# Performance work log

Measured on AMD Instinct MI355X. Metric: run time of the kernel, lower is better.

Reference implementation:

```python
import jax, jax.numpy as jnp
import numpy as np
from jax import lax

NH, K, V, TOPK = 8, 64, 64, 4  # n_heads, key_size, val_size, SparseAttention top_k(=3+1)
EPS = 1e-7
BN_EPS = 1e-5


def conv1x1(x, w, b):
    # x: [B,C,H,W], w: [O,C] -> [B,O,H,W]
    return jnp.einsum('oc,bchw->bohw', w, x) + b[None, :, None, None]


def conv3x3(x, w, b):
    y = lax.conv_general_dilated(x, w, (1, 1), 'SAME',
                                 dimension_numbers=('NCHW', 'OIHW', 'NCHW'))
    return y + b[None, :, None, None]


def batchnorm(x, g, b):
    # training-mode BN over (N,H,W), biased variance (matches torch BatchNorm2d in train)
    m = jnp.mean(x, axis=(0, 2, 3), keepdims=True)
    v = jnp.var(x, axis=(0, 2, 3), keepdims=True)
    return (x - m) * lax.rsqrt(v + BN_EPS) * g[None, :, None, None] + b[None, :, None, None]


def to_flat(y, d):
    # [B, NH*d, H, W] -> [B*H*W*NH, d]
    B, _, H, W = y.shape
    return y.reshape(B, NH, d, H, W).transpose(0, 3, 4, 1, 2).reshape(B * H * W * NH, d)


def setup_inputs() -> dict:
    key = jax.random.key(0)
    ks = jax.random.split(key, 16)
    L, C, B, H, W = 4, 256, 8, 32, 32
    KH, VH = K * NH, V * NH
    s = 0.02
    return {
        'x': jax.random.normal(ks[0], (B, C, H, W), jnp.float32),
        'kw': jax.random.normal(ks[1], (L, KH, C), jnp.float32) * s,
        'kb': jax.random.normal(ks[2], (L, KH), jnp.float32) * s,
        'qw': jax.random.normal(ks[3], (L, KH, C), jnp.float32) * s,
        'qb': jax.random.normal(ks[4], (L, KH), jnp.float32) * s,
        'vw': jax.random.normal(ks[5], (L, VH, C), jnp.float32) * s,
        'vb': jax.random.normal(ks[6], (L, VH), jnp.float32) * s,
        'ow1': jax.random.normal(ks[7], (L, C, VH, 3, 3), jnp.float32) * s,
        'ob1': jax.random.normal(ks[8], (L, C), jnp.float32) * s,
        'bn_g': jnp.ones((L, C), jnp.float32),
        'bn_b': jnp.zeros((L, C), jnp.float32),
        'ow2': jax.random.normal(ks[9], (L, C, C, 3, 3), jnp.float32) * s,
        'ob2': jax.random.normal(ks[10], (L, C), jnp.float32) * s,
        'gammas': jax.random.normal(ks[11], (L,), jnp.float32),
    }


def reference(x, kw, kb, qw, qb, vw, vb, ow1, ob1, bn_g, bn_b, ow2, ob2, gammas):
    B, C, H, W = x.shape
    L = kw.shape[0]
    temp = jnp.asarray(np.power(K, 0.5), x.dtype)  # concentration=0.5
    keys, vals = [], []
    for l in range(L):  # structurally distinct layers: growing key/val list
        keys.append(to_flat(conv1x1(x, kw[l], kb[l]), K))  # [N,K]
        vals.append(to_flat(conv1x1(x, vw[l], vb[l]), V))  # [N,V]
        q = to_flat(conv1x1(x, qw[l], qb[l]), K)           # [N,K]
        kt = jnp.stack(keys + [jnp.zeros_like(keys[0])], axis=1)  # [N,T,K] zero key appended
        vt = jnp.stack(vals + [jnp.zeros_like(vals[0])], axis=1)  # [N,T,V]
        scores = jnp.einsum('nk,ntk->nt', q / temp, kt)
        attn = jax.nn.softmax(scores, axis=-1)
        T = attn.shape[1]
        if T > TOPK:  # SparseAttention: topk threshold, clamp, renormalize
            delta = lax.top_k(attn, TOPK)[0][:, -1] + EPS
            wgt = jnp.maximum(attn - delta[:, None], 0.0)
            attn = wgt / (jnp.sum(wgt, axis=1, keepdims=True) + EPS)
        o = jnp.einsum('nt,ntv->nv', attn, vt)  # [N,V]
        o = o.reshape(B, H, W, NH * V).transpose(0, 3, 1, 2)  # [B, NH*V, H, W]
        h1 = jax.nn.relu(batchnorm(conv3x3(o, ow1[l], ob1[l]), bn_g[l], bn_b[l]))
        h2 = conv3x3(h1, ow2[l], ob2[l])
        x = x + h2 * gammas[l]
    return x
```

## Files before the change

### kernel.cpp

```cpp
#include <hip/hip_runtime.h>


typedef __attribute__((ext_vector_type(8))) short short8;
typedef __attribute__((ext_vector_type(4))) float f32x4;
typedef __attribute__((ext_vector_type(2))) float f32x2;
typedef __attribute__((ext_vector_type(4))) unsigned short ushort4_t;
typedef __attribute__((ext_vector_type(4))) unsigned int uint4_t;

#define NTOK 65536
#define NPIX 8192

#define PREP_FLAT 7752
#define PREP_W1   (PREP_FLAT + 1024)
#define PREP_W2   (PREP_W1 + 1024)
#define PREP_TOT  (PREP_W2 + 128)

__device__ __forceinline__ float bf2f(unsigned short u) {
  unsigned int v = ((unsigned int)u) << 16;
  float f; __builtin_memcpy(&f, &v, 4); return f;
}
__device__ __forceinline__ unsigned short f2bf(float f) {
  unsigned int u; __builtin_memcpy(&u, &f, 4);
  u = (u + 0x7FFFu + ((u >> 16) & 1u)) >> 16;
  return (unsigned short)u;
}
__device__ __forceinline__ float blo(unsigned int u) {
  unsigned int v = u << 16; float f; __builtin_memcpy(&f, &v, 4); return f;
}
__device__ __forceinline__ float bhi(unsigned int u) {
  unsigned int v = u & 0xFFFF0000u; float f; __builtin_memcpy(&f, &v, 4); return f;
}

__device__ __forceinline__ void gl_lds16(const unsigned short* g, const unsigned short* l) {
  __builtin_amdgcn_global_load_lds(
      (const __attribute__((address_space(1))) unsigned int*)g,
      (__attribute__((address_space(3))) unsigned int*)l, 16, 0, 0);
}

__global__ void k_prep(const float* __restrict__ kw, const float* __restrict__ vw,
                       const float* __restrict__ qw, const float* __restrict__ ow1,
                       const float* __restrict__ ow2, const float* __restrict__ kb,
                       const float* __restrict__ vb, const float* __restrict__ qb,
                       unsigned short* __restrict__ wkqv, unsigned short* __restrict__ w1,
                       unsigned short* __restrict__ w2, float* __restrict__ biascat,
                       unsigned int* __restrict__ opad_u32, unsigned int* __restrict__ h1pad_u32,
                       const float* __restrict__ x_in, float* __restrict__ xacc,
                       unsigned short* __restrict__ xcl) {
  const int bid = blockIdx.x;
  const int tid = threadIdx.x;

  if (bid < PREP_FLAT) {
    long i = (long)bid * 256 + tid;
    if (i < 1572864) {
      int idx = (int)(i & 131071); int sl = (int)(i >> 17); int slot = sl % 3, l = sl / 3;
      const float* s = slot == 0 ? kw : slot == 1 ? vw : qw;
      float v = s[(size_t)l * 131072 + idx];
      if (slot == 2) v *= 0.125f;
      wkqv[i] = f2bf(v);
      return;
    }
    i -= 1572864;
    if (i < 6144) {
      int o = (int)(i & 511); int sl = (int)(i >> 9); int slot = sl % 3, l = sl / 3;
      const float* s = slot == 0 ? kb : slot == 1 ? vb : qb;
      float v = s[l * 512 + o];
      if (slot == 2) v *= 0.125f;
      biascat[i] = v;
      return;
    }
    i -= 6144;
    auto border_pix = [](int pidx) -> size_t {
      const int b = pidx / 132, t = pidx % 132;
      int y, x;
      if (t < 34) { y = 0; x = t; }
      else if (t < 68) { y = 33; x = t - 34; }
      else { const int j = t - 68; y = 1 + (j >> 1); x = (j & 1) * 33; }
      return (size_t)b * 1156 + y * 34 + x;
    };
    if (i < 270336) {
      const int pidx = (int)(i >> 8), c = (int)(i & 255);
      opad_u32[border_pix(pidx) * 256 + c] = 0u;
      return;
    }
    i -= 270336;
    if (i < 135168) {
      const int pidx = (int)(i >> 7), c = (int)(i & 127);
      h1pad_u32[border_pix(pidx) * 128 + c] = 0u;
    }
    return;
  }

  if (bid < PREP_W1) {
    __shared__ unsigned short lds[4608];
    const int m = bid - PREP_FLAT;
    const float* src = ow1 + (size_t)m * 4608;
    #pragma unroll
    for (int k = 0; k < 18; k++) lds[k * 256 + tid] = f2bf(src[k * 256 + tid]);
    __syncthreads();
    unsigned int* dst = (unsigned int*)(w1 + (size_t)m * 4608);
    #pragma unroll
    for (int j = 0; j < 9; j++) {
      const int u = j * 256 + tid;
      const int o = 2 * u;
      const int tap = o >> 9, c = o & 511;
      dst[u] = (unsigned int)lds[c * 9 + tap] |
               ((unsigned int)lds[(c + 1) * 9 + tap] << 16);
    }
    return;
  }

  if (bid < PREP_W2) {
    __shared__ unsigned short lds2[2304];
    const int m = bid - PREP_W1;
    const float* src = ow2 + (size_t)m * 2304;
    #pragma unroll
    for (int k = 0; k < 9; k++) lds2[k * 256 + tid] = f2bf(src[k * 256 + tid]);
    __syncthreads();
    unsigned int* dst = (unsigned int*)(w2 + (size_t)m * 2304);
    #pragma unroll
    for (int j = 0; j < 5; j++) {
      const int u = j * 256 + tid;
      if (u < 1152) {
        const int o = 2 * u;
        const int tap = o >> 8, c = o & 255;
        dst[u] = (unsigned int)lds2[c * 9 + tap] |
                 ((unsigned int)lds2[(c + 1) * 9 + tap] << 16);
      }
    }
    return;
  }

  {
    __shared__ unsigned short t[64][68];
    const int xb = bid - PREP_W2;
    const int hw0 = (xb & 15) * 64, b = xb >> 4;
    for (int cc = 0; cc < 4; cc++) {
      __syncthreads();
      {
        const int px = tid & 63, c = tid >> 6;
        #pragma unroll
        for (int i = 0; i < 16; i++) {
          const size_t idx = ((size_t)b * 256 + cc * 64 + c + i * 4) * 1024 + hw0 + px;
          const float v = x_in[idx];
          xacc[idx] = v;
          t[px][c + i * 4] = f2bf(v);
        }
      }
      __syncthreads();
      {
        const int px = tid >> 2, c0 = (tid & 3) * 16;
        unsigned short* dp = xcl + ((size_t)b * 1024 + hw0 + px) * 256 + cc * 64 + c0;
        short8 v0, v1;
        #pragma unroll
        for (int i = 0; i < 8; i++) { v0[i] = (short)t[px][c0 + i]; v1[i] = (short)t[px][c0 + 8 + i]; }
        *(short8*)dp = v0; *(short8*)(dp + 8) = v1;
      }
    }
  }
}

template<int MODE, int NSTEP, int KDIM, int CIN, int NBUF>
__global__ __launch_bounds__(256) void k_gemm(
    const unsigned short* __restrict__ W,
    const unsigned short* __restrict__ act,
    const float* __restrict__ bias,
    int l,
    unsigned short* __restrict__ ktok, unsigned short* __restrict__ vtok,
    unsigned short* __restrict__ qtok,
    unsigned short* __restrict__ pout) {
  __shared__ unsigned short sm[NBUF][2][8192];

  const int bid = blockIdx.x;
  int m0, b, pix0, s;
  if constexpr (MODE == 0) {
    const int xcd = bid & 7, li = bid >> 3;
    const int nt = xcd * 8 + (li & 7);
    m0 = (li >> 3) * 128; s = 0;
    b = nt >> 3; pix0 = (nt & 7) * 128;
  } else {
    const int xcd = bid & 7, li = bid >> 3;
    const int nt = xcd * 8 + (li & 7);
    const int r = li >> 3;
    m0 = (r & 1) * 128; s = r >> 1;
    b = nt >> 3; pix0 = (nt & 7) * 128;
  }
  constexpr int SW = (MODE == 1) ? 128 : 64;

  const int tid = threadIdx.x;
  const int wid = tid >> 6, lane = tid & 63;
  const int lr = lane & 15, lg = lane >> 4;
  const int m_off = (wid >> 1) * 64, n_off = (wid & 1) * 64;

  const unsigned short* gA[4];
  const unsigned short* gB[4];
  #pragma unroll
  for (int j = 0; j < 4; j++) {
    const int o = (wid * 4 + j) * 512 + lane * 8;
    const int row = o >> 6;
    const int ksw = (((o >> 3) & 7) ^ (row & 7)) * 8;
    gA[j] = W + (size_t)(m0 + row) * KDIM + (MODE ? s * SW : 0) + ksw;
    if constexpr (MODE == 0) {
      gB[j] = act + ((size_t)b * 1024 + pix0 + row) * 256 + ksw;
    } else {
      const int pix = pix0 + row, py = pix >> 5, px = pix & 31;
      gB[j] = act + (size_t)b * 1156 * CIN + ((size_t)py * 34 + px) * CIN + s * SW + ksw;
    }
  }

  auto offA = [&](int st) -> int {
    if constexpr (MODE == 0) return st * 64;
    else if constexpr (MODE == 1) return (st >> 1) * 512 + (st & 1) * 64;
    else return st * 256;
  };
  auto offB = [&](int st) -> int {
    if constexpr (MODE == 0) return st * 64;
    else if constexpr (MODE == 1) {
      const int tap = st >> 1, dy = tap / 3, dx = tap - dy * 3;
      return (dy * 34 + dx) * 512 + (st & 1) * 64;
    } else {
      const int dy = st / 3, dx = st - dy * 3;
      return (dy * 34 + dx) * 256;
    }
  };
  auto STAGE = [&](int bf, int st) {
    const int oa = offA(st), ob = offB(st);
    #pragma unroll
    for (int j = 0; j < 4; j++) gl_lds16(gA[j] + oa, &sm[bf][0][(wid * 4 + j) * 512]);
    #pragma unroll
    for (int j = 0; j < 4; j++) gl_lds16(gB[j] + ob, &sm[bf][1][(wid * 4 + j) * 512]);
  };
  auto COMPUTE = [&](int cur, f32x4 (*acc)[4]) {
    #pragma unroll
    for (int ks = 0; ks < 2; ks++) {
      short8 af[4], bfr[4];
      #pragma unroll
      for (int i = 0; i < 4; i++) {
        const int ra = m_off + i * 16 + lr;
        af[i] = *(const short8*)&sm[cur][0][ra * 64 + (((ks * 4 + lg) ^ (ra & 7)) * 8)];
        const int rb = n_off + i * 16 + lr;
        bfr[i] = *(const short8*)&sm[cur][1][rb * 64 + (((ks * 4 + lg) ^ (rb & 7)) * 8)];
      }
      #pragma unroll
      for (int i = 0; i < 4; i++)
        #pragma unroll
        for (int jn = 0; jn < 4; jn++)
          acc[i][jn] = __builtin_amdgcn_mfma_f32_16x16x32_bf16(af[i], bfr[jn], acc[i][jn], 0, 0, 0);
    }
  };

  f32x4 acc[4][4] = {};

  if constexpr (NBUF == 2) {
    STAGE(0, 0);
    __syncthreads();
    #pragma unroll
    for (int st = 0; st < NSTEP; st++) {
      if (st + 1 < NSTEP) STAGE((st + 1) & 1, st + 1);
      COMPUTE(st & 1, acc);
      __syncthreads();
    }
  } else {
    #pragma unroll
    for (int st = 0; st < NSTEP; st++) {
      if (st) __syncthreads();
      STAGE(0, st);
      __syncthreads();
      COMPUTE(0, acc);
    }
  }

  if constexpr (MODE == 0) {
    #pragma unroll
    for (int mi = 0; mi < 4; mi++) {
      const int mb = m0 + m_off + mi * 16 + lg * 4;
      const int tensor = mb >> 9, head = (mb >> 6) & 7, d0 = mb & 63;
      unsigned short* dst = (tensor == 0) ? ktok + (size_t)l * NTOK * 64
                          : (tensor == 1) ? vtok + (size_t)l * NTOK * 64 : qtok;
      const float b0 = bias[mb], b1 = bias[mb + 1], b2 = bias[mb + 2], b3 = bias[mb + 3];
      #pragma unroll
      for (int ni = 0; ni < 4; ni++) {
        const int n = pix0 + n_off + ni * 16 + lr;
        ushort4_t pk;
        pk[0] = f2bf(acc[mi][ni][0] + b0); pk[1] = f2bf(acc[mi][ni][1] + b1);
        pk[2] = f2bf(acc[mi][ni][2] + b2); pk[3] = f2bf(acc[mi][ni][3] + b3);
        *(ushort4_t*)&dst[(((size_t)b * 1024 + n) * 8 + head) * 64 + d0] = pk;
      }
    }
  } else {
    #pragma unroll
    for (int mi = 0; mi < 4; mi++) {
      const int mb = m0 + m_off + mi * 16 + lg * 4;
      unsigned short* orow = pout + (size_t)(s * 256 + mb) * 8192 + (size_t)b * 1024 + pix0;
      #pragma unroll
      for (int ni = 0; ni < 4; ni++) {
        const int n = n_off + ni * 16 + lr;
        #pragma unroll
        for (int r = 0; r < 4; r++) orow[(size_t)r * 8192 + n] = f2bf(acc[mi][ni][r]);
      }
    }
  }
}

template<int L>
__global__ __launch_bounds__(256) void k_attn(const unsigned int* __restrict__ q_tok,
                                              const unsigned int* __restrict__ k_tok,
                                              const unsigned int* __restrict__ v_tok,
                                              unsigned int* __restrict__ opad) {
  constexpr int T = L + 2;
  const int lane = threadIdx.x & 63, wid = threadIdx.x >> 6;
  const int ti = lane >> 2, dq = lane & 3;
  const int token = blockIdx.x * 64 + wid * 16 + ti;
  const size_t rowq = (size_t)token * 32 + dq * 8;

  unsigned int q[8];
  *(uint4_t*)&q[0] = *(const uint4_t*)(q_tok + rowq);
  *(uint4_t*)&q[4] = *(const uint4_t*)(q_tok + rowq + 4);
  float qf[16];
  #pragma unroll
  for (int j = 0; j < 8; j++) {
    qf[2 * j]     = blo(q[j]);
    qf[2 * j + 1] = bhi(q[j]);
  }

  float s[T];
  s[T - 1] = 0.0f;
  #pragma unroll
  for (int t = 0; t <= L; t++) {
    const unsigned int* kp = k_tok + (size_t)t * (NTOK * 32) + rowq;
    unsigned int kk[8];
    *(uint4_t*)&kk[0] = *(const uint4_t*)kp;
    *(uint4_t*)&kk[4] = *(const uint4_t*)(kp + 4);
    float p = 0.0f;
    #pragma unroll
    for (int j = 0; j < 8; j++) {
      p = fmaf(qf[2 * j], blo(kk[j]), p);
      p = fmaf(qf[2 * j + 1], bhi(kk[j]), p);
    }
    p += __shfl_xor(p, 1);
    p += __shfl_xor(p, 2);
    s[t] = p;
  }

  float mx = s[0];
  #pragma unroll
  for (int t = 1; t < T; t++) mx = fmaxf(mx, s[t]);
  float attn[T], sum = 0.0f;
  #pragma unroll
  for (int t = 0; t < T; t++) { attn[t] = __expf(s[t] - mx); sum += attn[t]; }
  const float inv = 1.0f / sum;
  #pragma unroll
  for (int t = 0; t < T; t++) attn[t] *= inv;

  if constexpr (T == 5) {
    float m1 = attn[0], m2 = 1e30f;
    #pragma unroll
    for (int t = 1; t < 5; t++) {
      const float a = attn[t];
      const float nm1 = fminf(m1, a);
      m2 = fminf(m2, fmaxf(m1, a));
      m1 = nm1;
    }
    const float delta = m2 + 1e-7f;
    float ws = 0.0f;
    #pragma unroll
    for (int t = 0; t < 5; t++) { attn[t] = fmaxf(attn[t] - delta, 0.0f); ws += attn[t]; }
    const float r = 1.0f / (ws + 1e-7f);
    #pragma unroll
    for (int t = 0; t < 5; t++) attn[t] *= r;
  }

  float o[16];
  #pragma unroll
  for (int i = 0; i < 16; i++) o[i] = 0.0f;
  #pragma unroll
  for (int t = 0; t <= L; t++) {
    const unsigned int* vp = v_tok + (size_t)t * (NTOK * 32) + rowq;
    unsigned int vv[8];
    *(uint4_t*)&vv[0] = *(const uint4_t*)vp;
    *(uint4_t*)&vv[4] = *(const uint4_t*)(vp + 4);
    const float a = attn[t];
    #pragma unroll
    for (int j = 0; j < 8; j++) {
      o[2 * j]     = fmaf(a, blo(vv[j]), o[2 * j]);
      o[2 * j + 1] = fmaf(a, bhi(vv[j]), o[2 * j + 1]);
    }
  }

  unsigned int po[8];
  #pragma unroll
  for (int j = 0; j < 8; j++) {
    unsigned int r;
    asm("v_cvt_pk_bf16_f32 %0, %1, %2" : "=v"(r) : "v"(o[2 * j]), "v"(o[2 * j + 1]));
    po[j] = r;
  }
  const int head = token & 7, pix = token >> 3;
  const int b = pix >> 10, hw = pix & 1023, y = hw >> 5, x = hw & 31;
  unsigned int* dp = opad +
      (((size_t)b * 1156 + (y + 1) * 34 + (x + 1)) * 512 + head * 64 + dq * 16) / 2;
  *(uint4_t*)dp = *(uint4_t*)&po[0];
  *(uint4_t*)(dp + 4) = *(uint4_t*)&po[4];
}

__global__ __launch_bounds__(512) void k_comb_stats(const unsigned int* __restrict__ p,
    const float* __restrict__ bias1, const float* __restrict__ g, const float* __restrict__ bta,
    float* __restrict__ stats) {
  const int c = blockIdx.x, tid = threadIdx.x;
  const float bs = bias1[c];
  const unsigned int* P0 = p + (size_t)c * 4096;
  float s = 0.0f, ss = 0.0f;
  #pragma unroll
  for (int k2 = 0; k2 < 2; k2++) {
    const int j = (k2 * 512 + tid) * 4;
    uint4_t a0 = *(const uint4_t*)(P0 + j);
    uint4_t a1 = *(const uint4_t*)(P0 + 1048576 + j);
    uint4_t a2 = *(const uint4_t*)(P0 + 2097152 + j);
    uint4_t a3 = *(const uint4_t*)(P0 + 3145728 + j);
    #pragma unroll
    for (int e = 0; e < 4; e++) {
      const float vl = blo(a0[e]) + blo(a1[e]) + blo(a2[e]) + blo(a3[e]) + bs;
      const float vh = bhi(a0[e]) + bhi(a1[e]) + bhi(a2[e]) + bhi(a3[e]) + bs;
      s += vl + vh; ss += vl * vl + vh * vh;
    }
  }
  #pragma unroll
  for (int o2 = 32; o2 > 0; o2 >>= 1) { s += __shfl_xor(s, o2); ss += __shfl_xor(ss, o2); }
  __shared__ float rs[8], rss[8];
  const int wid = tid >> 6, lane = tid & 63;
  if (lane == 0) { rs[wid] = s; rss[wid] = ss; }
  __syncthreads();
  if (tid == 0) {
    float S = 0.0f, SS = 0.0f;
    #pragma unroll
    for (int w = 0; w < 8; w++) { S += rs[w]; SS += rss[w]; }
    const float m = S * (1.0f / 8192.0f);
    const float var = SS * (1.0f / 8192.0f) - m * m;
    const float A = g[c] * rsqrtf(var + 1e-5f);
    stats[c] = A;
    stats[256 + c] = bta[c] - m * A;
  }
}

__global__ __launch_bounds__(512) void k_bn_relu_pad(const unsigned int* __restrict__ p,
    const float* __restrict__ bias1, const float* __restrict__ stats,
    unsigned short* __restrict__ hpad) {
  __shared__ unsigned short t[32][264];
  const int hw0 = blockIdx.x * 32, b = blockIdx.y, tid = threadIdx.x;
  const int u = tid & 15, cg = tid >> 4;
  const int base = ((b * 1024 + hw0) >> 1);
  #pragma unroll
  for (int i = 0; i < 8; i++) {
    const int ch = i * 32 + cg;
    const float bs = bias1[ch];
    const float A = stats[ch], Bt = stats[256 + ch];
    const size_t j = (size_t)ch * 4096 + base + u;
    const unsigned int a0 = p[j];
    const unsigned int a1 = p[j + 1048576];
    const unsigned int a2 = p[j + 2097152];
    const unsigned int a3 = p[j + 3145728];
    const float vl = blo(a0) + blo(a1) + blo(a2) + blo(a3) + bs;
    const float vh = bhi(a0) + bhi(a1) + bhi(a2) + bhi(a3) + bs;
    t[2 * u][ch]     = f2bf(fmaxf(vl * A + Bt, 0.0f));
    t[2 * u + 1][ch] = f2bf(fmaxf(vh * A + Bt, 0.0f));
  }
  __syncthreads();
  const int px = tid >> 4, c0 = (tid & 15) * 16;
  const int y = hw0 >> 5, x = hw0 & 31;
  unsigned short* dp = hpad + ((size_t)b * 1156 + (y + 1) * 34 + (x + px + 1)) * 256 + c0;
  short8 v0, v1;
  #pragma unroll
  for (int i = 0; i < 8; i++) { v0[i] = (short)t[px][c0 + i]; v1[i] = (short)t[px][c0 + 8 + i]; }
  *(short8*)dp = v0; *(short8*)(dp + 8) = v1;
}

__global__ __launch_bounds__(512) void k_comb2(const unsigned int* __restrict__ p,
    const float* __restrict__ bias2, const float* __restrict__ gamma_p, int last,
    float* __restrict__ xacc, unsigned short* __restrict__ xcl) {
  __shared__ unsigned short t[32][264];
  const int hw0 = blockIdx.x * 32, b = blockIdx.y, tid = threadIdx.x;
  const int u = tid & 15, cg = tid >> 4;
  const float gmm = gamma_p[0];
  const int base = ((b * 1024 + hw0) >> 1);
  #pragma unroll
  for (int i = 0; i < 8; i++) {
    const int ch = i * 32 + cg;
    const float bs = bias2[ch];
    const size_t j = (size_t)ch * 4096 + base + u;
    const unsigned int a0 = p[j];
    const unsigned int a1 = p[j + 1048576];
    const unsigned int a2 = p[j + 2097152];
    const unsigned int a3 = p[j + 3145728];
    const float vl = blo(a0) + blo(a1) + blo(a2) + blo(a3) + bs;
    const float vh = bhi(a0) + bhi(a1) + bhi(a2) + bhi(a3) + bs;
    float* X = xacc + ((size_t)b * 256 + ch) * 1024 + hw0 + 2 * u;
    f32x2 xv = *(const f32x2*)X;
    const float xl = xv[0] + gmm * vl;
    const float xh = xv[1] + gmm * vh;
    f32x2 xw = {xl, xh};
    *(f32x2*)X = xw;
    t[2 * u][ch]     = f2bf(xl);
    t[2 * u + 1][ch] = f2bf(xh);
  }
  __syncthreads();
  if (!last) {
    const int px = tid >> 4, c0 = (tid & 15) * 16;
    unsigned short* dp = xcl + ((size_t)b * 1024 + hw0 + px) * 256 + c0;
    short8 v0, v1;
    #pragma unroll
    for (int i = 0; i < 8; i++) { v0[i] = (short)t[px][c0 + i]; v1[i] = (short)t[px][c0 + 8 + i]; }
    *(short8*)dp = v0; *(short8*)(dp + 8) = v1;
  }
}

extern "C" void kernel_launch(void* const* d_in, const int* in_sizes, int n_in,
                              void* d_out, int out_size, void* d_ws, size_t ws_size,
                              hipStream_t stream) {
  (void)in_sizes; (void)n_in; (void)out_size;
  const float* x_in   = (const float*)d_in[0];
  const float* kw     = (const float*)d_in[1];
  const float* kb     = (const float*)d_in[2];
  const float* qw     = (const float*)d_in[3];
  const float* qb     = (const float*)d_in[4];
  const float* vw     = (const float*)d_in[5];
  const float* vb     = (const float*)d_in[6];
  const float* ow1    = (const float*)d_in[7];
  const float* ob1    = (const float*)d_in[8];
  const float* bn_g   = (const float*)d_in[9];
  const float* bn_b   = (const float*)d_in[10];
  const float* ow2    = (const float*)d_in[11];
  const float* ob2    = (const float*)d_in[12];
  const float* gammas = (const float*)d_in[13];

  char* ws = (char*)d_ws;
  size_t off = 0;
  auto alloc = [&](size_t bytes) -> void* {
    void* pp = ws + off;
    off += (bytes + 255) & ~(size_t)255;
    return pp;
  };
  unsigned short* xcl     = (unsigned short*)alloc((size_t)NPIX * 256 * 2);
  unsigned short* k_tok   = (unsigned short*)alloc((size_t)4 * NTOK * 64 * 2);
  unsigned short* v_tok   = (unsigned short*)alloc((size_t)4 * NTOK * 64 * 2);
  unsigned short* q_tok   = (unsigned short*)alloc((size_t)NTOK * 64 * 2);
  unsigned short* opad    = (unsigned short*)alloc((size_t)8 * 1156 * 512 * 2);
  unsigned short* h1pad   = (unsigned short*)alloc((size_t)8 * 1156 * 256 * 2);
  unsigned short* p1      = (unsigned short*)alloc((size_t)4 * 256 * 8192 * 2);
  float*          stats   = (float*)alloc(512 * 4);
  unsigned short* wkqv    = (unsigned short*)alloc((size_t)4 * 3 * 512 * 256 * 2);
  unsigned short* w1bf    = (unsigned short*)alloc((size_t)1024 * 4608 * 2);
  unsigned short* w2bf    = (unsigned short*)alloc((size_t)1024 * 2304 * 2);
  float*          biascat = (float*)alloc((size_t)6144 * 4);
  if (off > ws_size) return;

  float* xacc = (float*)d_out;

  k_prep<<<PREP_TOT, 256, 0, stream>>>(
      kw, vw, qw, ow1, ow2, kb, vb, qb,
      wkqv, w1bf, w2bf, biascat,
      (unsigned int*)opad, (unsigned int*)h1pad,
      x_in, xacc, xcl);

  for (int l = 0; l < 4; l++) {
    k_gemm<0, 4, 256, 256, 1><<<768, 256, 0, stream>>>(
        wkqv + (size_t)l * 3 * 512 * 256, xcl, biascat + l * 1536, l,
        k_tok, v_tok, q_tok, nullptr);
    const unsigned int* qt = (const unsigned int*)q_tok;
    const unsigned int* kt = (const unsigned int*)k_tok;
    const unsigned int* vt = (const unsigned int*)v_tok;
    unsigned int* op = (unsigned int*)opad;
    switch (l) {
      case 0: k_attn<0><<<1024, 256, 0, stream>>>(qt, kt, vt, op); break;
      case 1: k_attn<1><<<1024, 256, 0, stream>>>(qt, kt, vt, op); break;
      case 2: k_attn<2><<<1024, 256, 0, stream>>>(qt, kt, vt, op); break;
      default: k_attn<3><<<1024, 256, 0, stream>>>(qt, kt, vt, op); break;
    }
    k_gemm<1, 18, 4608, 512, 2><<<512, 256, 0, stream>>>(
        w1bf + (size_t)l * 256 * 4608, opad, nullptr, l,
        nullptr, nullptr, nullptr, p1);
    k_comb_stats<<<256, 512, 0, stream>>>((const unsigned int*)p1, ob1 + l * 256,
                                          bn_g + l * 256, bn_b + l * 256, stats);
    k_bn_relu_pad<<<dim3(32, 8), 512, 0, stream>>>((const unsigned int*)p1,
                                                   ob1 + l * 256, stats, h1pad);
    k_gemm<2, 9, 2304, 256, 2><<<512, 256, 0, stream>>>(
        w2bf + (size_t)l * 256 * 2304, h1pad, nullptr, l,
        nullptr, nullptr, nullptr, p1);
    k_comb2<<<dim3(32, 8), 512, 0, stream>>>((const unsigned int*)p1, ob2 + l * 256,
                                             gammas + l, (l == 3) ? 1 : 0, xacc, xcl);
  }
}
```

Baseline: 349.4 us.

## Switch GEMM kernel to 32x32x16 MFMA with chunk-major LDS layout

Replaces the 16x16x32 bf16 MFMA tiles (4x4 per wave) with 32x32x16 MFMA tiles (2x2 per wave), which halves the number of LDS fragment loads per k-step. The LDS staging layout changes from an XOR-swizzled row-major form to a chunk-major layout in which each 8-element k chunk of all 128 rows is contiguous, so the larger-tile fragment reads are linear per lane. The epilogues are rewritten for the 32x32 accumulator layout. Dropping the swizzle may change LDS bank-conflict behaviour, and the new global-to-LDS gather uses per-row 16-byte strided loads.

```diff
diff --git a/kernel.cpp b/kernel.cpp
--- a/kernel.cpp
+++ b/kernel.cpp
@@ -2,7 +2,7 @@
 
 
 typedef __attribute__((ext_vector_type(8))) short short8;
-typedef __attribute__((ext_vector_type(4))) float f32x4;
+typedef __attribute__((ext_vector_type(16))) float f32x16;
 typedef __attribute__((ext_vector_type(2))) float f32x2;
 typedef __attribute__((ext_vector_type(4))) unsigned short ushort4_t;
 typedef __attribute__((ext_vector_type(4))) unsigned int uint4_t;
@@ -188,22 +188,22 @@
 
   const int tid = threadIdx.x;
   const int wid = tid >> 6, lane = tid & 63;
-  const int lr = lane & 15, lg = lane >> 4;
+  const int l31 = lane & 31, hi = lane >> 5;
   const int m_off = (wid >> 1) * 64, n_off = (wid & 1) * 64;
 
   const unsigned short* gA[4];
   const unsigned short* gB[4];
   #pragma unroll
   for (int j = 0; j < 4; j++) {
-    const int o = (wid * 4 + j) * 512 + lane * 8;
-    const int row = o >> 6;
-    const int ksw = (((o >> 3) & 7) ^ (row & 7)) * 8;
-    gA[j] = W + (size_t)(m0 + row) * KDIM + (MODE ? s * SW : 0) + ksw;
+    const int idx = wid * 4 + j;
+    const int chunk = idx >> 1;
+    const int row = (idx & 1) * 64 + lane;
+    gA[j] = W + (size_t)(m0 + row) * KDIM + (MODE ? s * SW : 0) + chunk * 8;
     if constexpr (MODE == 0) {
-      gB[j] = act + ((size_t)b * 1024 + pix0 + row) * 256 + ksw;
+      gB[j] = act + ((size_t)b * 1024 + pix0 + row) * 256 + chunk * 8;
     } else {
       const int pix = pix0 + row, py = pix >> 5, px = pix & 31;
-      gB[j] = act + (size_t)b * 1156 * CIN + ((size_t)py * 34 + px) * CIN + s * SW + ksw;
+      gB[j] = act + (size_t)b * 1156 * CIN + ((size_t)py * 34 + px) * CIN + s * SW + chunk * 8;
     }
   }
 
@@ -229,26 +229,26 @@
     #pragma unroll
     for (int j = 0; j < 4; j++) gl_lds16(gB[j] + ob, &sm[bf][1][(wid * 4 + j) * 512]);
   };
-  auto COMPUTE = [&](int cur, f32x4 (*acc)[4]) {
-    #pragma unroll
-    for (int ks = 0; ks < 2; ks++) {
-      short8 af[4], bfr[4];
-      #pragma unroll
-      for (int i = 0; i < 4; i++) {
-        const int ra = m_off + i * 16 + lr;
-        af[i] = *(const short8*)&sm[cur][0][ra * 64 + (((ks * 4 + lg) ^ (ra & 7)) * 8)];
-        const int rb = n_off + i * 16 + lr;
-        bfr[i] = *(const short8*)&sm[cur][1][rb * 64 + (((ks * 4 + lg) ^ (rb & 7)) * 8)];
-      }
-      #pragma unroll
-      for (int i = 0; i < 4; i++)
-        #pragma unroll
-        for (int jn = 0; jn < 4; jn++)
-          acc[i][jn] = __builtin_amdgcn_mfma_f32_16x16x32_bf16(af[i], bfr[jn], acc[i][jn], 0, 0, 0);
+
+  const int ard0 = (m_off + l31) * 8,      ard1 = (m_off + 32 + l31) * 8;
+  const int brd0 = (n_off + l31) * 8,      brd1 = (n_off + 32 + l31) * 8;
+
+  f32x16 acc[2][2] = {};
+
+  auto COMPUTE = [&](int cur) {
+    #pragma unroll
+    for (int ks = 0; ks < 4; ks++) {
+      const int co = (ks * 2 + hi) * 1024;
+      short8 a0 = *(const short8*)&sm[cur][0][co + ard0];
+      short8 a1 = *(const short8*)&sm[cur][0][co + ard1];
+      short8 b0 = *(const short8*)&sm[cur][1][co + brd0];
+      short8 b1 = *(const short8*)&sm[cur][1][co + brd1];
+      acc[0][0] = __builtin_amdgcn_mfma_f32_32x32x16_bf16(a0, b0, acc[0][0], 0, 0, 0);
+      acc[0][1] = __builtin_amdgcn_mfma_f32_32x32x16_bf16(a0, b1, acc[0][1], 0, 0, 0);
+      acc[1][0] = __builtin_amdgcn_mfma_f32_32x32x16_bf16(a1, b0, acc[1][0], 0, 0, 0);
+      acc[1][1] = __builtin_amdgcn_mfma_f32_32x32x16_bf16(a1, b1, acc[1][1], 0, 0, 0);
     }
   };
-
-  f32x4 acc[4][4] = {};
 
   if constexpr (NBUF == 2) {
     STAGE(0, 0);
@@ -256,7 +256,7 @@
     #pragma unroll
     for (int st = 0; st < NSTEP; st++) {
       if (st + 1 < NSTEP) STAGE((st + 1) & 1, st + 1);
-      COMPUTE(st & 1, acc);
+      COMPUTE(st & 1);
       __syncthreads();
     }
   } else {
@@ -265,37 +265,47 @@
       if (st) __syncthreads();
       STAGE(0, st);
       __syncthreads();
-      COMPUTE(0, acc);
+      COMPUTE(0);
     }
   }
 
   if constexpr (MODE == 0) {
     #pragma unroll
-    for (int mi = 0; mi < 4; mi++) {
-      const int mb = m0 + m_off + mi * 16 + lg * 4;
-      const int tensor = mb >> 9, head = (mb >> 6) & 7, d0 = mb & 63;
+    for (int mi = 0; mi < 2; mi++) {
+      const int mbase = m0 + m_off + mi * 32;
+      const int tensor = mbase >> 9, head = (mbase >> 6) & 7, d0b = mbase & 63;
       unsigned short* dst = (tensor == 0) ? ktok + (size_t)l * NTOK * 64
                           : (tensor == 1) ? vtok + (size_t)l * NTOK * 64 : qtok;
-      const float b0 = bias[mb], b1 = bias[mb + 1], b2 = bias[mb + 2], b3 = bias[mb + 3];
       #pragma unroll
-      for (int ni = 0; ni < 4; ni++) {
-        const int n = pix0 + n_off + ni * 16 + lr;
-        ushort4_t pk;
-        pk[0] = f2bf(acc[mi][ni][0] + b0); pk[1] = f2bf(acc[mi][ni][1] + b1);
-        pk[2] = f2bf(acc[mi][ni][2] + b2); pk[3] = f2bf(acc[mi][ni][3] + b3);
-        *(ushort4_t*)&dst[(((size_t)b * 1024 + n) * 8 + head) * 64 + d0] = pk;
+      for (int ni = 0; ni < 2; ni++) {
+        const int n = pix0 + n_off + ni * 32 + l31;
+        unsigned short* tokp = dst + (((size_t)b * 1024 + n) * 8 + head) * 64;
+        #pragma unroll
+        for (int q = 0; q < 4; q++) {
+          const int rowoff = 8 * q + 4 * hi;
+          const int m4 = mbase + rowoff;
+          ushort4_t pk;
+          #pragma unroll
+          for (int e = 0; e < 4; e++) pk[e] = f2bf(acc[mi][ni][q * 4 + e] + bias[m4 + e]);
+          *(ushort4_t*)&tokp[d0b + rowoff] = pk;
+        }
       }
     }
   } else {
     #pragma unroll
-    for (int mi = 0; mi < 4; mi++) {
-      const int mb = m0 + m_off + mi * 16 + lg * 4;
-      unsigned short* orow = pout + (size_t)(s * 256 + mb) * 8192 + (size_t)b * 1024 + pix0;
+    for (int mi = 0; mi < 2; mi++) {
+      const int mbase = m0 + m_off + mi * 32;
       #pragma unroll
-      for (int ni = 0; ni < 4; ni++) {
-        const int n = n_off + ni * 16 + lr;
+      for (int ni = 0; ni < 2; ni++) {
+        const int n = n_off + ni * 32 + l31;
         #pragma unroll
-        for (int r = 0; r < 4; r++) orow[(size_t)r * 8192 + n] = f2bf(acc[mi][ni][r]);
+        for (int q = 0; q < 4; q++) {
+          const int rowoff = 8 * q + 4 * hi;
+          unsigned short* orow = pout + (size_t)(s * 256 + mbase + rowoff) * 8192
+                               + (size_t)b * 1024 + pix0 + n;
+          #pragma unroll
+          for (int e = 0; e < 4; e++) orow[(size_t)e * 8192] = f2bf(acc[mi][ni][q * 4 + e]);
+        }
       }
     }
   }
```

Result: slower. 500.7 us (+43.3%).
